# Optimization experiments

Hardware: AMD Instinct MI355X
Metric: run time of the kernel (lower is better)

Reference implementation:

```python
import jax, jax.numpy as jnp
import numpy as np

N_NODES = 200000
IN_DIM = 128
HID = 256
OUT = 128
B = 2048
K = 16  # sampled temporal fanout per hop


def setup_inputs() -> dict:
    rng = np.random.default_rng(0)
    x = rng.standard_normal((N_NODES, IN_DIM), dtype=np.float32)
    batch = rng.integers(0, N_NODES, size=B).astype(np.int32)
    ts = rng.uniform(0.5, 1.0, size=B).astype(np.float32)

    # hop 1: K temporal neighbors per seed node, edge times <= query time
    nbr1 = rng.integers(0, N_NODES, size=B * K).astype(np.int32)
    t_edge1 = (rng.uniform(0.0, 1.0, size=(B, K)) * ts[:, None]).astype(np.float32)
    n_times1 = t_edge1.max(axis=1)                       # [B] max neighbor time per seed
    seg1 = np.repeat(np.arange(B, dtype=np.int32), K)    # [E1]

    # second-level frontier: neighbors first, then the batch itself
    nodes2 = np.concatenate([nbr1, batch])               # [N2 = B*K + B]
    t2 = np.concatenate([t_edge1.reshape(-1), ts]).astype(np.float32)
    N2 = nodes2.shape[0]

    # hop 2
    nbr2 = rng.integers(0, N_NODES, size=N2 * K).astype(np.int32)
    t_edge2 = (rng.uniform(0.0, 1.0, size=(N2, K)) * t2[:, None]).astype(np.float32)
    n_times2 = t_edge2.max(axis=1)                       # [N2]
    seg2 = np.repeat(np.arange(N2, dtype=np.int32), K)   # [E2]

    def lin(ko, fan_out, fan_in):
        lim = 1.0 / np.sqrt(fan_in)
        kw, kb = jax.random.split(ko)
        W = jax.random.uniform(kw, (fan_out, fan_in), jnp.float32, -lim, lim)
        b = jax.random.uniform(kb, (fan_out,), jnp.float32, -lim, lim)
        return W, b

    key = jax.random.key(0)
    k1, k2, k3, k4, k5 = jax.random.split(key, 5)
    W1n, b1n = lin(k1, HID, IN_DIM)
    W1h, b1h = lin(k2, HID, IN_DIM)
    W2n, b2n = lin(k3, OUT, HID)
    W2h, b2h = lin(k4, OUT, HID)
    t_kernel = jax.random.uniform(k5, (1,), jnp.float32)

    return {
        "x": jnp.asarray(x), "ts": jnp.asarray(ts), "t2": jnp.asarray(t2),
        "n_times1": jnp.asarray(n_times1), "n_times2": jnp.asarray(n_times2),
        "W1n": W1n, "b1n": b1n, "W1h": W1h, "b1h": b1h,
        "W2n": W2n, "b2n": b2n, "W2h": W2h, "b2h": b2h,
        "t_kernel": t_kernel,
        "nodes2": jnp.asarray(nodes2), "nbr2": jnp.asarray(nbr2),
        "seg2": jnp.asarray(seg2), "seg1": jnp.asarray(seg1),
    }


def reference(x, ts, t2, n_times1, n_times2, W1n, b1n, W1h, b1h,
              W2n, b2n, W2h, b2h, t_kernel, nodes2, nbr2, seg2, seg1):
    N2 = nodes2.shape[0]
    Bn = ts.shape[0]
    E1 = N2 - Bn

    def decay(dt):  # exp(-t_kernel * dt), t_kernel shape (1,) broadcasts
        return jnp.exp(-t_kernel * dt)

    # ---- layer 1 (inner recursion; layer-0 embeddings are raw features x) ----
    agg2 = jax.ops.segment_sum(x[nbr2], seg2, num_segments=N2)   # [N2, D] neighbor sums
    hn1 = x[nodes2] * decay(t2 - n_times2)[:, None]              # self feats * temporal decay
    h1 = jax.nn.relu(agg2 @ W1n.T + b1n + hn1 @ W1h.T + b1h)     # [N2, HID]

    # ---- layer 2 (top) ----
    agg1 = jax.ops.segment_sum(h1[:E1], seg1, num_segments=Bn)   # [B, HID]
    hn2 = h1[E1:] * decay(ts - n_times1)[:, None]                # [B, HID]
    out = jax.nn.relu(agg1 @ W2n.T + b2n + hn2 @ W2h.T + b2h)    # [B, OUT]
    return out
```

## Files before the change

### kernel.cpp

```cpp
#include <hip/hip_runtime.h>
#include <hip/hip_bf16.h>

#define N2V    34816
#define BATCH  2048
#define E1V    32768
#define KFAN   16
#define INDIM  128
#define HID    256
#define OUTD   128

#define OFF_BS1   0
#define OFF_BS2   256
#define OFF_WC1B  384
#define OFF_WC2B  33152
#define OFF_ZG    65920
#define OFF_AGG1B 4522368
#define OFF_H1S   4784512

#define GATHER_BLOCKS (N2V / 16)

typedef __attribute__((ext_vector_type(8))) short bf16x8;
typedef __attribute__((ext_vector_type(4))) short short4v;
typedef __attribute__((ext_vector_type(4))) float f32x4;

__device__ __forceinline__ float bf2f(short u) {
  union { unsigned u32; float f; } cv;
  cv.u32 = ((unsigned)(unsigned short)u) << 16;
  return cv.f;
}

__device__ __forceinline__ short f2b(float f) {
  __hip_bfloat16 h = __float2bfloat16(f);
  return *reinterpret_cast<short*>(&h);
}

__global__ __launch_bounds__(256) void gather_prepack_kernel(
    const float* __restrict__ x, const float* __restrict__ t2,
    const float* __restrict__ n_times2, const int* __restrict__ nodes2,
    const int* __restrict__ nbr2, const float* __restrict__ tk,
    const float* __restrict__ W1n, const float* __restrict__ b1n,
    const float* __restrict__ W1h, const float* __restrict__ b1h,
    const float* __restrict__ W2n, const float* __restrict__ b2n,
    const float* __restrict__ W2h, const float* __restrict__ b2h,
    __hip_bfloat16* __restrict__ zg,
    __hip_bfloat16* __restrict__ Wc1b, __hip_bfloat16* __restrict__ Wc2b,
    float* __restrict__ bs1, float* __restrict__ bs2) {
  const int t = threadIdx.x;
  if (blockIdx.x >= GATHER_BLOCKS) {
    int idx = (blockIdx.x - GATHER_BLOCKS) * 256 + t;
    int j1 = idx >> 8, c1 = idx & 255;
    float v1 = (c1 < 128) ? W1n[j1 * 128 + c1] : W1h[j1 * 128 + (c1 - 128)];
    Wc1b[idx] = __float2bfloat16(v1);
    int j2 = idx >> 9, c2 = idx & 511;
    float v2 = (c2 < 256) ? W2n[j2 * 256 + c2] : W2h[j2 * 256 + (c2 - 256)];
    Wc2b[idx] = __float2bfloat16(v2);
    if (idx < 256) bs1[idx] = b1n[idx] + b1h[idx];
    if (idx < 128) bs2[idx] = b2n[idx] + b2h[idx];
    return;
  }

  const int i = blockIdx.x * 16 + (t >> 4);
  const int c = t & 15;
  const float4* __restrict__ x4 = (const float4*)x;

  const int4* nb4 = reinterpret_cast<const int4*>(nbr2) + i * 4;
  int4 n0 = nb4[0], n1 = nb4[1], n2 = nb4[2], n3 = nb4[3];
  const int idx[16] = {n0.x, n0.y, n0.z, n0.w, n1.x, n1.y, n1.z, n1.w,
                       n2.x, n2.y, n2.z, n2.w, n3.x, n3.y, n3.z, n3.w};

  float4 s0 = {0.f, 0.f, 0.f, 0.f};
  float4 s1 = {0.f, 0.f, 0.f, 0.f};
#pragma unroll
  for (int k = 0; k < KFAN; ++k) {
    const float4* rp = x4 + (size_t)idx[k] * 32;
    float4 v0 = rp[c];
    float4 v1 = rp[16 + c];
    s0.x += v0.x; s0.y += v0.y; s0.z += v0.z; s0.w += v0.w;
    s1.x += v1.x; s1.y += v1.y; s1.z += v1.z; s1.w += v1.w;
  }
  const float dec = __expf(-tk[0] * (t2[i] - n_times2[i]));
  const float4* sp = x4 + (size_t)nodes2[i] * 32;
  float4 u0 = sp[c];
  float4 u1 = sp[16 + c];

  char* rowp = (char*)zg + (size_t)i * 512;
  short4v p;
  p = (short4v){f2b(s0.x), f2b(s0.y), f2b(s0.z), f2b(s0.w)};
  *reinterpret_cast<short4v*>(rowp + c * 8) = p;
  p = (short4v){f2b(s1.x), f2b(s1.y), f2b(s1.z), f2b(s1.w)};
  *reinterpret_cast<short4v*>(rowp + 128 + c * 8) = p;
  p = (short4v){f2b(u0.x * dec), f2b(u0.y * dec), f2b(u0.z * dec), f2b(u0.w * dec)};
  *reinterpret_cast<short4v*>(rowp + 256 + c * 8) = p;
  p = (short4v){f2b(u1.x * dec), f2b(u1.y * dec), f2b(u1.z * dec), f2b(u1.w * dec)};
  *reinterpret_cast<short4v*>(rowp + 384 + c * 8) = p;
}

__global__ __launch_bounds__(256) void gemm1_kernel(
    const __hip_bfloat16* __restrict__ zg,
    const __hip_bfloat16* __restrict__ Wc1b,
    const float* __restrict__ bs1,
    __hip_bfloat16* __restrict__ agg1b, __hip_bfloat16* __restrict__ h1s) {
  __shared__ __hip_bfloat16 z[32][264];
  const int t = threadIdx.x;
  const int i0 = blockIdx.x * 32;

  const char* src = (const char*)zg + (size_t)i0 * 512;
#pragma unroll
  for (int it = 0; it < 4; ++it) {
    int o = it * 4096 + t * 16;
    int row = o >> 9, colb = o & 511;
    bf16x8 v = *reinterpret_cast<const bf16x8*>(src + o);
    *reinterpret_cast<bf16x8*>((char*)&z[0][0] + row * 528 + colb) = v;
  }
  __syncthreads();

  const int wid = t >> 6;
  const int lane = t & 63;
  const int lr = lane & 15;
  const int lk8 = (lane >> 4) * 8;
  const int ncol0 = wid * 64;
  const short* __restrict__ wsrc = (const short*)Wc1b;

  f32x4 acc[2][4];
#pragma unroll
  for (int m = 0; m < 2; ++m)
#pragma unroll
    for (int n = 0; n < 4; ++n) acc[m][n] = (f32x4){0.f, 0.f, 0.f, 0.f};

#pragma unroll
  for (int ks = 0; ks < 8; ++ks) {
    const int kb = ks * 32 + lk8;
    bf16x8 a0 = *reinterpret_cast<const bf16x8*>((char*)&z[0][0] + lr * 528 + kb * 2);
    bf16x8 a1 = *reinterpret_cast<const bf16x8*>((char*)&z[0][0] + (16 + lr) * 528 + kb * 2);
#pragma unroll
    for (int nt = 0; nt < 4; ++nt) {
      bf16x8 b = *reinterpret_cast<const bf16x8*>(
          wsrc + (size_t)(ncol0 + nt * 16 + lr) * 256 + kb);
      acc[0][nt] = __builtin_amdgcn_mfma_f32_16x16x32_bf16(a0, b, acc[0][nt], 0, 0, 0);
      acc[1][nt] = __builtin_amdgcn_mfma_f32_16x16x32_bf16(a1, b, acc[1][nt], 0, 0, 0);
    }
  }

  if (i0 < E1V) {
#pragma unroll
    for (int nt = 0; nt < 4; ++nt) {
      const int col = ncol0 + nt * 16 + lr;
      const float bias = bs1[col];
#pragma unroll
      for (int mt = 0; mt < 2; ++mt) {
        float v = 0.f;
#pragma unroll
        for (int q = 0; q < 4; ++q) v += fmaxf(acc[mt][nt][q] + bias, 0.f);
        v += __shfl_xor(v, 16);
        v += __shfl_xor(v, 32);
        if (lane < 16) {
          const int seg = (i0 >> 4) + mt;
          agg1b[(size_t)seg * HID + col] = __float2bfloat16(v);
        }
      }
    }
  } else {
    const int orow = (lane >> 4) * 4;
#pragma unroll
    for (int nt = 0; nt < 4; ++nt) {
      const int col = ncol0 + nt * 16 + lr;
      const float bias = bs1[col];
#pragma unroll
      for (int mt = 0; mt < 2; ++mt) {
#pragma unroll
        for (int q = 0; q < 4; ++q) {
          const int row = i0 + mt * 16 + orow + q;
          h1s[(size_t)(row - E1V) * HID + col] =
              __float2bfloat16(fmaxf(acc[mt][nt][q] + bias, 0.f));
        }
      }
    }
  }
}

__global__ __launch_bounds__(64) void layer2_kernel(
    const __hip_bfloat16* __restrict__ agg1b, const __hip_bfloat16* __restrict__ h1s,
    const float* __restrict__ ts, const float* __restrict__ n_times1,
    const float* __restrict__ tk, const __hip_bfloat16* __restrict__ Wc2b,
    const float* __restrict__ bs2, float* __restrict__ out) {
  const int lane = threadIdx.x;
  const int b0 = blockIdx.x * 16;
  const int lr = lane & 15;
  const int lk8 = (lane >> 4) * 8;
  const int row = b0 + lr;

  const float dec = __expf(-tk[0] * (ts[row] - n_times1[row]));
  const short* __restrict__ ag = (const short*)agg1b;
  const short* __restrict__ hs = (const short*)h1s;
  const short* __restrict__ w2 = (const short*)Wc2b;

  f32x4 acc[8];
#pragma unroll
  for (int n = 0; n < 8; ++n) acc[n] = (f32x4){0.f, 0.f, 0.f, 0.f};

#pragma unroll
  for (int ks = 0; ks < 16; ++ks) {
    const int kb = ks * 32 + lk8;
    bf16x8 a;
    if (kb < HID) {
      a = *reinterpret_cast<const bf16x8*>(ag + (size_t)row * HID + kb);
    } else {
      bf16x8 hv = *reinterpret_cast<const bf16x8*>(hs + (size_t)row * HID + (kb - HID));
#pragma unroll
      for (int e = 0; e < 8; ++e) a[e] = f2b(bf2f(hv[e]) * dec);
    }
#pragma unroll
    for (int nt = 0; nt < 8; ++nt) {
      bf16x8 b = *reinterpret_cast<const bf16x8*>(
          w2 + (size_t)(nt * 16 + lr) * 512 + kb);
      acc[nt] = __builtin_amdgcn_mfma_f32_16x16x32_bf16(a, b, acc[nt], 0, 0, 0);
    }
  }

  const int orow = (lane >> 4) * 4;
#pragma unroll
  for (int nt = 0; nt < 8; ++nt) {
    const int col = nt * 16 + lr;
    const float bias = bs2[col];
#pragma unroll
    for (int q = 0; q < 4; ++q) {
      out[(size_t)(b0 + orow + q) * OUTD + col] = fmaxf(acc[nt][q] + bias, 0.f);
    }
  }
}

extern "C" void kernel_launch(void* const* d_in, const int* in_sizes, int n_in,
                              void* d_out, int out_size, void* d_ws, size_t ws_size,
                              hipStream_t stream) {
  const float* x        = (const float*)d_in[0];
  const float* ts       = (const float*)d_in[1];
  const float* t2       = (const float*)d_in[2];
  const float* n_times1 = (const float*)d_in[3];
  const float* n_times2 = (const float*)d_in[4];
  const float* W1n      = (const float*)d_in[5];
  const float* b1n      = (const float*)d_in[6];
  const float* W1h      = (const float*)d_in[7];
  const float* b1h      = (const float*)d_in[8];
  const float* W2n      = (const float*)d_in[9];
  const float* b2n      = (const float*)d_in[10];
  const float* W2h      = (const float*)d_in[11];
  const float* b2h      = (const float*)d_in[12];
  const float* tk       = (const float*)d_in[13];
  const int*   nodes2   = (const int*)d_in[14];
  const int*   nbr2     = (const int*)d_in[15];

  float* ws = (float*)d_ws;
  float* bs1 = ws + OFF_BS1;
  float* bs2 = ws + OFF_BS2;
  __hip_bfloat16* Wc1b  = (__hip_bfloat16*)(ws + OFF_WC1B);
  __hip_bfloat16* Wc2b  = (__hip_bfloat16*)(ws + OFF_WC2B);
  __hip_bfloat16* zg    = (__hip_bfloat16*)(ws + OFF_ZG);
  __hip_bfloat16* agg1b = (__hip_bfloat16*)(ws + OFF_AGG1B);
  __hip_bfloat16* h1s   = (__hip_bfloat16*)(ws + OFF_H1S);
  float* out = (float*)d_out;

  gather_prepack_kernel<<<GATHER_BLOCKS + 256, 256, 0, stream>>>(
      x, t2, n_times2, nodes2, nbr2, tk,
      W1n, b1n, W1h, b1h, W2n, b2n, W2h, b2h,
      zg, Wc1b, Wc2b, bs1, bs2);
  gemm1_kernel<<<N2V / 32, 256, 0, stream>>>(zg, Wc1b, bs1, agg1b, h1s);
  layer2_kernel<<<BATCH / 16, 64, 0, stream>>>(agg1b, h1s, ts, n_times1, tk,
                                               Wc2b, bs2, out);
}
```

Measured before the change: 88.61 us.

## Fuse neighbor gather into layer-1 GEMM via shared memory staging

The gather/decay stage now writes its bf16 rows into shared memory and the same block runs the layer-1 MFMA GEMM, so the global zg intermediate buffer and its round trip are removed. Weight prepacking moves to a separate small kernel, and the GEMM tile shrinks from 32 to 16 rows per block. In exchange, each block re-reads the weight tile for half as many rows, and the gather latency is no longer overlapped with other blocks' GEMM work through a kernel boundary.

```diff
diff --git a/kernel.cpp b/kernel.cpp
--- a/kernel.cpp
+++ b/kernel.cpp
@@ -13,11 +13,8 @@
 #define OFF_BS2   256
 #define OFF_WC1B  384
 #define OFF_WC2B  33152
-#define OFF_ZG    65920
-#define OFF_AGG1B 4522368
-#define OFF_H1S   4784512
-
-#define GATHER_BLOCKS (N2V / 16)
+#define OFF_AGG1B 65920
+#define OFF_H1S   328064
 
 typedef __attribute__((ext_vector_type(8))) short bf16x8;
 typedef __attribute__((ext_vector_type(4))) short short4v;
@@ -34,83 +31,69 @@
   return *reinterpret_cast<short*>(&h);
 }
 
-__global__ __launch_bounds__(256) void gather_prepack_kernel(
-    const float* __restrict__ x, const float* __restrict__ t2,
-    const float* __restrict__ n_times2, const int* __restrict__ nodes2,
-    const int* __restrict__ nbr2, const float* __restrict__ tk,
+__global__ __launch_bounds__(256) void prepack_kernel(
     const float* __restrict__ W1n, const float* __restrict__ b1n,
     const float* __restrict__ W1h, const float* __restrict__ b1h,
     const float* __restrict__ W2n, const float* __restrict__ b2n,
     const float* __restrict__ W2h, const float* __restrict__ b2h,
-    __hip_bfloat16* __restrict__ zg,
     __hip_bfloat16* __restrict__ Wc1b, __hip_bfloat16* __restrict__ Wc2b,
     float* __restrict__ bs1, float* __restrict__ bs2) {
+  int idx = blockIdx.x * 256 + threadIdx.x;
+  int j1 = idx >> 8, c1 = idx & 255;
+  float v1 = (c1 < 128) ? W1n[j1 * 128 + c1] : W1h[j1 * 128 + (c1 - 128)];
+  Wc1b[idx] = __float2bfloat16(v1);
+  int j2 = idx >> 9, c2 = idx & 511;
+  float v2 = (c2 < 256) ? W2n[j2 * 256 + c2] : W2h[j2 * 256 + (c2 - 256)];
+  Wc2b[idx] = __float2bfloat16(v2);
+  if (idx < 256) bs1[idx] = b1n[idx] + b1h[idx];
+  if (idx < 128) bs2[idx] = b2n[idx] + b2h[idx];
+}
+
+__global__ __launch_bounds__(256) void fused1_kernel(
+    const float* __restrict__ x, const float* __restrict__ t2,
+    const float* __restrict__ n_times2, const int* __restrict__ nodes2,
+    const int* __restrict__ nbr2, const float* __restrict__ tk,
+    const __hip_bfloat16* __restrict__ Wc1b, const float* __restrict__ bs1,
+    __hip_bfloat16* __restrict__ agg1b, __hip_bfloat16* __restrict__ h1s) {
+  __shared__ __hip_bfloat16 z[16][264];
   const int t = threadIdx.x;
-  if (blockIdx.x >= GATHER_BLOCKS) {
-    int idx = (blockIdx.x - GATHER_BLOCKS) * 256 + t;
-    int j1 = idx >> 8, c1 = idx & 255;
-    float v1 = (c1 < 128) ? W1n[j1 * 128 + c1] : W1h[j1 * 128 + (c1 - 128)];
-    Wc1b[idx] = __float2bfloat16(v1);
-    int j2 = idx >> 9, c2 = idx & 511;
-    float v2 = (c2 < 256) ? W2n[j2 * 256 + c2] : W2h[j2 * 256 + (c2 - 256)];
-    Wc2b[idx] = __float2bfloat16(v2);
-    if (idx < 256) bs1[idx] = b1n[idx] + b1h[idx];
-    if (idx < 128) bs2[idx] = b2n[idx] + b2h[idx];
-    return;
-  }
-
-  const int i = blockIdx.x * 16 + (t >> 4);
-  const int c = t & 15;
-  const float4* __restrict__ x4 = (const float4*)x;
-
-  const int4* nb4 = reinterpret_cast<const int4*>(nbr2) + i * 4;
-  int4 n0 = nb4[0], n1 = nb4[1], n2 = nb4[2], n3 = nb4[3];
-  const int idx[16] = {n0.x, n0.y, n0.z, n0.w, n1.x, n1.y, n1.z, n1.w,
-                       n2.x, n2.y, n2.z, n2.w, n3.x, n3.y, n3.z, n3.w};
-
-  float4 s0 = {0.f, 0.f, 0.f, 0.f};
-  float4 s1 = {0.f, 0.f, 0.f, 0.f};
-#pragma unroll
-  for (int k = 0; k < KFAN; ++k) {
-    const float4* rp = x4 + (size_t)idx[k] * 32;
-    float4 v0 = rp[c];
-    float4 v1 = rp[16 + c];
-    s0.x += v0.x; s0.y += v0.y; s0.z += v0.z; s0.w += v0.w;
-    s1.x += v1.x; s1.y += v1.y; s1.z += v1.z; s1.w += v1.w;
-  }
-  const float dec = __expf(-tk[0] * (t2[i] - n_times2[i]));
-  const float4* sp = x4 + (size_t)nodes2[i] * 32;
-  float4 u0 = sp[c];
-  float4 u1 = sp[16 + c];
-
-  char* rowp = (char*)zg + (size_t)i * 512;
-  short4v p;
-  p = (short4v){f2b(s0.x), f2b(s0.y), f2b(s0.z), f2b(s0.w)};
-  *reinterpret_cast<short4v*>(rowp + c * 8) = p;
-  p = (short4v){f2b(s1.x), f2b(s1.y), f2b(s1.z), f2b(s1.w)};
-  *reinterpret_cast<short4v*>(rowp + 128 + c * 8) = p;
-  p = (short4v){f2b(u0.x * dec), f2b(u0.y * dec), f2b(u0.z * dec), f2b(u0.w * dec)};
-  *reinterpret_cast<short4v*>(rowp + 256 + c * 8) = p;
-  p = (short4v){f2b(u1.x * dec), f2b(u1.y * dec), f2b(u1.z * dec), f2b(u1.w * dec)};
-  *reinterpret_cast<short4v*>(rowp + 384 + c * 8) = p;
-}
-
-__global__ __launch_bounds__(256) void gemm1_kernel(
-    const __hip_bfloat16* __restrict__ zg,
-    const __hip_bfloat16* __restrict__ Wc1b,
-    const float* __restrict__ bs1,
-    __hip_bfloat16* __restrict__ agg1b, __hip_bfloat16* __restrict__ h1s) {
-  __shared__ __hip_bfloat16 z[32][264];
-  const int t = threadIdx.x;
-  const int i0 = blockIdx.x * 32;
-
-  const char* src = (const char*)zg + (size_t)i0 * 512;
-#pragma unroll
-  for (int it = 0; it < 4; ++it) {
-    int o = it * 4096 + t * 16;
-    int row = o >> 9, colb = o & 511;
-    bf16x8 v = *reinterpret_cast<const bf16x8*>(src + o);
-    *reinterpret_cast<bf16x8*>((char*)&z[0][0] + row * 528 + colb) = v;
+  const int i0 = blockIdx.x * 16;
+  {
+    const int r = t >> 4;
+    const int c = t & 15;
+    const int i = i0 + r;
+    const float4* __restrict__ x4 = (const float4*)x;
+
+    const int4* nb4 = reinterpret_cast<const int4*>(nbr2) + i * 4;
+    int4 n0 = nb4[0], n1 = nb4[1], n2 = nb4[2], n3 = nb4[3];
+    const int idx[16] = {n0.x, n0.y, n0.z, n0.w, n1.x, n1.y, n1.z, n1.w,
+                         n2.x, n2.y, n2.z, n2.w, n3.x, n3.y, n3.z, n3.w};
+
+    float4 s0 = {0.f, 0.f, 0.f, 0.f};
+    float4 s1 = {0.f, 0.f, 0.f, 0.f};
+#pragma unroll
+    for (int k = 0; k < KFAN; ++k) {
+      const float4* rp = x4 + (size_t)idx[k] * 32;
+      float4 v0 = rp[c];
+      float4 v1 = rp[16 + c];
+      s0.x += v0.x; s0.y += v0.y; s0.z += v0.z; s0.w += v0.w;
+      s1.x += v1.x; s1.y += v1.y; s1.z += v1.z; s1.w += v1.w;
+    }
+    const float dec = __expf(-tk[0] * (t2[i] - n_times2[i]));
+    const float4* sp = x4 + (size_t)nodes2[i] * 32;
+    float4 u0 = sp[c];
+    float4 u1 = sp[16 + c];
+
+    char* zrow = (char*)&z[0][0] + r * 528;
+    short4v p;
+    p = (short4v){f2b(s0.x), f2b(s0.y), f2b(s0.z), f2b(s0.w)};
+    *reinterpret_cast<short4v*>(zrow + c * 8) = p;
+    p = (short4v){f2b(s1.x), f2b(s1.y), f2b(s1.z), f2b(s1.w)};
+    *reinterpret_cast<short4v*>(zrow + 128 + c * 8) = p;
+    p = (short4v){f2b(u0.x * dec), f2b(u0.y * dec), f2b(u0.z * dec), f2b(u0.w * dec)};
+    *reinterpret_cast<short4v*>(zrow + 256 + c * 8) = p;
+    p = (short4v){f2b(u1.x * dec), f2b(u1.y * dec), f2b(u1.z * dec), f2b(u1.w * dec)};
+    *reinterpret_cast<short4v*>(zrow + 384 + c * 8) = p;
   }
   __syncthreads();
 
@@ -121,23 +104,19 @@
   const int ncol0 = wid * 64;
   const short* __restrict__ wsrc = (const short*)Wc1b;
 
-  f32x4 acc[2][4];
-#pragma unroll
-  for (int m = 0; m < 2; ++m)
-#pragma unroll
-    for (int n = 0; n < 4; ++n) acc[m][n] = (f32x4){0.f, 0.f, 0.f, 0.f};
+  f32x4 acc[4];
+#pragma unroll
+  for (int n = 0; n < 4; ++n) acc[n] = (f32x4){0.f, 0.f, 0.f, 0.f};
 
 #pragma unroll
   for (int ks = 0; ks < 8; ++ks) {
     const int kb = ks * 32 + lk8;
-    bf16x8 a0 = *reinterpret_cast<const bf16x8*>((char*)&z[0][0] + lr * 528 + kb * 2);
-    bf16x8 a1 = *reinterpret_cast<const bf16x8*>((char*)&z[0][0] + (16 + lr) * 528 + kb * 2);
+    bf16x8 a = *reinterpret_cast<const bf16x8*>((char*)&z[0][0] + lr * 528 + kb * 2);
 #pragma unroll
     for (int nt = 0; nt < 4; ++nt) {
       bf16x8 b = *reinterpret_cast<const bf16x8*>(
           wsrc + (size_t)(ncol0 + nt * 16 + lr) * 256 + kb);
-      acc[0][nt] = __builtin_amdgcn_mfma_f32_16x16x32_bf16(a0, b, acc[0][nt], 0, 0, 0);
-      acc[1][nt] = __builtin_amdgcn_mfma_f32_16x16x32_bf16(a1, b, acc[1][nt], 0, 0, 0);
+      acc[nt] = __builtin_amdgcn_mfma_f32_16x16x32_bf16(a, b, acc[nt], 0, 0, 0);
     }
   }
 
@@ -146,17 +125,13 @@
     for (int nt = 0; nt < 4; ++nt) {
       const int col = ncol0 + nt * 16 + lr;
       const float bias = bs1[col];
-#pragma unroll
-      for (int mt = 0; mt < 2; ++mt) {
-        float v = 0.f;
-#pragma unroll
-        for (int q = 0; q < 4; ++q) v += fmaxf(acc[mt][nt][q] + bias, 0.f);
-        v += __shfl_xor(v, 16);
-        v += __shfl_xor(v, 32);
-        if (lane < 16) {
-          const int seg = (i0 >> 4) + mt;
-          agg1b[(size_t)seg * HID + col] = __float2bfloat16(v);
-        }
+      float v = 0.f;
+#pragma unroll
+      for (int q = 0; q < 4; ++q) v += fmaxf(acc[nt][q] + bias, 0.f);
+      v += __shfl_xor(v, 16);
+      v += __shfl_xor(v, 32);
+      if (lane < 16) {
+        agg1b[(size_t)blockIdx.x * HID + col] = __float2bfloat16(v);
       }
     }
   } else {
@@ -166,13 +141,10 @@
       const int col = ncol0 + nt * 16 + lr;
       const float bias = bs1[col];
 #pragma unroll
-      for (int mt = 0; mt < 2; ++mt) {
-#pragma unroll
-        for (int q = 0; q < 4; ++q) {
-          const int row = i0 + mt * 16 + orow + q;
-          h1s[(size_t)(row - E1V) * HID + col] =
-              __float2bfloat16(fmaxf(acc[mt][nt][q] + bias, 0.f));
-        }
+      for (int q = 0; q < 4; ++q) {
+        const int row = i0 - E1V + orow + q;
+        h1s[(size_t)row * HID + col] =
+            __float2bfloat16(fmaxf(acc[nt][q] + bias, 0.f));
       }
     }
   }
@@ -254,16 +226,15 @@
   float* bs2 = ws + OFF_BS2;
   __hip_bfloat16* Wc1b  = (__hip_bfloat16*)(ws + OFF_WC1B);
   __hip_bfloat16* Wc2b  = (__hip_bfloat16*)(ws + OFF_WC2B);
-  __hip_bfloat16* zg    = (__hip_bfloat16*)(ws + OFF_ZG);
   __hip_bfloat16* agg1b = (__hip_bfloat16*)(ws + OFF_AGG1B);
   __hip_bfloat16* h1s   = (__hip_bfloat16*)(ws + OFF_H1S);
   float* out = (float*)d_out;
 
-  gather_prepack_kernel<<<GATHER_BLOCKS + 256, 256, 0, stream>>>(
-      x, t2, n_times2, nodes2, nbr2, tk,
-      W1n, b1n, W1h, b1h, W2n, b2n, W2h, b2h,
-      zg, Wc1b, Wc2b, bs1, bs2);
-  gemm1_kernel<<<N2V / 32, 256, 0, stream>>>(zg, Wc1b, bs1, agg1b, h1s);
+  prepack_kernel<<<256, 256, 0, stream>>>(W1n, b1n, W1h, b1h,
+                                          W2n, b2n, W2h, b2h,
+                                          Wc1b, Wc2b, bs1, bs2);
+  fused1_kernel<<<N2V / 16, 256, 0, stream>>>(x, t2, n_times2, nodes2, nbr2, tk,
+                                              Wc1b, bs1, agg1b, h1s);
   layer2_kernel<<<BATCH / 16, 64, 0, stream>>>(agg1b, h1s, ts, n_times1, tk,
                                                Wc2b, bs2, out);
 }
```

Result: faster. 77.21 us, median of 3 (-12.9%).
